# Kernel tuning notes

Hardware: AMD Instinct MI355X
Metric: run time of the kernel (lower is better)

Reference implementation:

```python
import jax, jax.numpy as jnp
import numpy as np

WS = 7        # window size (cubic)
SHIFT = 3     # shift size (cubic)
NH = 6        # num heads
EPS = 1e-5


def _layernorm(x, g, b):
    m = x.mean(-1, keepdims=True)
    v = ((x - m) ** 2).mean(-1, keepdims=True)
    return (x - m) / jnp.sqrt(v + EPS) * g + b


def _win_partition(x, ws):
    # (B,H,W,T,C) -> (B*nW, ws^3, C)
    B, H, W, T, C = x.shape
    x = x.reshape(B, H // ws, ws, W // ws, ws, T // ws, ws, C)
    return x.transpose(0, 1, 3, 5, 2, 4, 6, 7).reshape(-1, ws * ws * ws, C)


def _win_reverse(w, ws, B, H, W, T):
    # (B*nW, ws^3, C) -> (B,H,W,T,C)
    C = w.shape[-1]
    x = w.reshape(B, H // ws, W // ws, T // ws, ws, ws, ws, C)
    return x.transpose(0, 1, 4, 2, 5, 3, 6, 7).reshape(B, H, W, T, C)


def _rel_index(ws):
    # 3D relative position index, (N, N) int, N = ws^3 (torch.meshgrid default 'ij')
    coords = np.stack(np.meshgrid(np.arange(ws), np.arange(ws), np.arange(ws), indexing='ij'))
    cf = coords.reshape(3, -1)
    rel = (cf[:, :, None] - cf[:, None, :]).transpose(1, 2, 0)
    rel[:, :, 0] += ws - 1
    rel[:, :, 1] += ws - 1
    rel[:, :, 2] += ws - 1
    rel[:, :, 0] *= (2 * ws - 1) ** 2
    rel[:, :, 1] *= (2 * ws - 1)
    return rel.sum(-1)


def _compute_mask(Hp, Wp, Tp, ws, shift):
    img = np.zeros((1, Hp, Wp, Tp, 1), np.float32)
    cnt = 0
    sl = (slice(0, -ws), slice(-ws, -shift), slice(-shift, None))
    for h in sl:
        for w in sl:
            for t in sl:
                img[:, h, w, t, :] = cnt
                cnt += 1
    mw = np.asarray(_win_partition(jnp.asarray(img), ws)).reshape(-1, ws ** 3)  # (nW, N)
    am = mw[:, None, :] - mw[:, :, None]
    return jnp.asarray(np.where(am != 0, -100.0, 0.0).astype(np.float32))


def setup_inputs() -> dict:
    key = jax.random.key(0)
    ks = jax.random.split(key, 10)
    B, Hd, Wd, Td, C = 2, 28, 28, 28, 192
    L = Hd * Wd * Td
    Ch = int(C * 4.0)
    s = 0.02
    inp = {
        'x': jax.random.normal(ks[0], (B, L, C), jnp.float32),
        'mask': _compute_mask(Hd, Wd, Td, WS, SHIFT),
        'gamma1': jnp.ones((C,), jnp.float32),
        'beta1': jnp.zeros((C,), jnp.float32),
        'qkv_w': jax.random.normal(ks[1], (3 * C, C), jnp.float32) * s,
        'qkv_b': jnp.zeros((3 * C,), jnp.float32),
        'rpb_table': jax.random.normal(ks[2], ((2 * WS - 1) ** 3, NH), jnp.float32) * s,
        'proj_w': jax.random.normal(ks[3], (C, C), jnp.float32) * s,
        'proj_b': jnp.zeros((C,), jnp.float32),
        'gamma2': jnp.ones((C,), jnp.float32),
        'beta2': jnp.zeros((C,), jnp.float32),
        'fc1_w': jax.random.normal(ks[4], (Ch, C), jnp.float32) * s,
        'fc1_b': jnp.zeros((Ch,), jnp.float32),
        'fc2_w': jax.random.normal(ks[5], (C, Ch), jnp.float32) * s,
        'fc2_b': jnp.zeros((C,), jnp.float32),
        'H': Hd, 'W': Wd, 'T': Td,
    }
    return inp


def reference(x, mask, gamma1, beta1, qkv_w, qkv_b, rpb_table, proj_w, proj_b,
              gamma2, beta2, fc1_w, fc1_b, fc2_w, fc2_b, H, W, T):
    B, L, C = x.shape
    hd = C // NH
    scale = hd ** -0.5
    shortcut = x

    h1 = _layernorm(x, gamma1, beta1).reshape(B, H, W, T, C)
    # H,W,T are multiples of WS -> no padding; cyclic shift for SW-MSA
    shifted = jnp.roll(h1, (-SHIFT, -SHIFT, -SHIFT), axis=(1, 2, 3))
    xw = _win_partition(shifted, WS)            # (B*nW, N, C)
    Bn, N, _ = xw.shape

    qkv = (xw @ qkv_w.T + qkv_b).reshape(Bn, N, 3, NH, hd).transpose(2, 0, 3, 1, 4)
    q, k, v = qkv[0] * scale, qkv[1], qkv[2]     # (Bn, NH, N, hd)
    attn = jnp.einsum('bhnd,bhmd->bhnm', q, k)   # (Bn, NH, N, N)

    idx = _rel_index(WS)
    bias = rpb_table[idx.reshape(-1)].reshape(N, N, NH).transpose(2, 0, 1)
    attn = attn + bias[None]

    nW = mask.shape[0]
    attn = attn.reshape(Bn // nW, nW, NH, N, N) + mask[None, :, None]
    attn = jax.nn.softmax(attn.reshape(Bn, NH, N, N), axis=-1)

    out = jnp.einsum('bhnm,bhmd->bhnd', attn, v).transpose(0, 2, 1, 3).reshape(Bn, N, C)
    out = out @ proj_w.T + proj_b

    shifted = _win_reverse(out, WS, B, H, W, T)
    xr = jnp.roll(shifted, (SHIFT, SHIFT, SHIFT), axis=(1, 2, 3)).reshape(B, L, C)

    x = shortcut + xr
    h2 = _layernorm(x, gamma2, beta2)
    m = jax.nn.gelu(h2 @ fc1_w.T + fc1_b, approximate=False)
    return x + (m @ fc2_w.T + fc2_b)
```

## Files before the change

kernel.cpp:

```cpp
#include <hip/hip_runtime.h>
#include <hip/hip_bf16.h>

typedef unsigned short u16;
typedef unsigned int u32;
typedef __attribute__((ext_vector_type(8))) short s16x8;
typedef __attribute__((ext_vector_type(4))) float f32x4;

__device__ __forceinline__ u16 f2bf(float f) {
    union { float f; u32 u; } x; x.f = f;
    u32 r = x.u + 0x7fffu + ((x.u >> 16) & 1u);
    return (u16)(r >> 16);
}
__device__ __forceinline__ float bflo(u32 v) {
    union { u32 u; float f; } x; x.u = v << 16; return x.f;
}
__device__ __forceinline__ float bfhi(u32 v) {
    union { u32 u; float f; } x; x.u = v & 0xffff0000u; return x.f;
}
__device__ __forceinline__ u32 cvt_pk_bf16(float a, float b) {
    u32 r;
    asm("v_cvt_pk_bf16_f32 %0, %1, %2" : "=v"(r) : "v"(a), "v"(b));
    return r;
}
__device__ __forceinline__ void gl2lds(const u16* g, u16* l) {
    __builtin_amdgcn_global_load_lds(
        (const __attribute__((address_space(1))) unsigned int*)g,
        (__attribute__((address_space(3))) unsigned int*)l, 16, 0, 0);
}

#define L_TOK 21952
#define C_DIM 192
#define LOG2E 1.4426950408889634f
#define Q2SCALE 0.2550565444463649f
#define BT_STR 352

__global__ __launch_bounds__(256) void cvt_k(const float* __restrict__ s0,
                                             const float* __restrict__ s1,
                                             const float* __restrict__ s2,
                                             const float* __restrict__ s3,
                                             u16* __restrict__ dst)
{
    int i = blockIdx.x * 256 + threadIdx.x;
    float v;
    if (i < 110592) v = s0[i];
    else if (i < 147456) v = s1[i - 110592];
    else if (i < 294912) v = s2[i - 147456];
    else v = s3[i - 294912];
    dst[i] = f2bf(v);
}

__global__ __launch_bounds__(256) void bias48_k(const float* __restrict__ rpb,
                                                u16* __restrict__ biasT)
{
    const int gid = blockIdx.x * 256 + threadIdx.x;
    const int z = gid / 30976;
    const int rem = gid - z * 30976;
    const int m = rem / 88;
    const int n0 = (rem - m * 88) * 4;
    const int hh = z >> 3, wt = z & 7;

    u16 v[4];
    if (m <= 342) {
        const int hm = m / 49, r2 = m - hm * 49, wm = r2 / 7, tm = r2 - wm * 7;
        const int rm = ((wt & 4) ? (hm < 4 ? 1 : 2) : 0) * 9
                     + ((wt & 2) ? (wm < 4 ? 1 : 2) : 0) * 3
                     + ((wt & 1) ? (tm < 4 ? 1 : 2) : 0);
        #pragma unroll
        for (int j = 0; j < 4; j++) {
            const int n = n0 + j;
            float b = -100000.0f;
            if (n <= 342) {
                int hq = n / 49, r1 = n - hq * 49, wq = r1 / 7, tq = r1 - wq * 7;
                int idx = ((hq - hm + 6) * 13 + (wq - wm + 6)) * 13 + (tq - tm + 6);
                b = rpb[idx * 6 + hh];
                int rq = ((wt & 4) ? (hq < 4 ? 1 : 2) : 0) * 9
                       + ((wt & 2) ? (wq < 4 ? 1 : 2) : 0) * 3
                       + ((wt & 1) ? (tq < 4 ? 1 : 2) : 0);
                if (rq != rm) b -= 100.0f;
                b *= LOG2E;
            }
            v[j] = f2bf(b);
        }
    } else {
        const u16 neg = f2bf(-100000.0f);
        v[0] = neg; v[1] = neg; v[2] = neg; v[3] = neg;
    }
    u32 lo = (u32)v[0] | ((u32)v[1] << 16);
    u32 hi = (u32)v[2] | ((u32)v[3] << 16);
    *(uint2*)&biasT[((size_t)z * 352 + m) * BT_STR + n0] = (uint2){lo, hi};
}

template<int MODE>
__global__ __launch_bounds__(256) void ln_k(const float* __restrict__ in,
                                            const float* __restrict__ g,
                                            const float* __restrict__ b,
                                            u16* __restrict__ out)
{
    const int lane = threadIdx.x & 63, wv = threadIdx.x >> 6;
    const int tok = blockIdx.x * 4 + wv;
    size_t base = (size_t)tok * C_DIM;
    float x0 = in[base + lane];
    float x1 = in[base + 64 + lane];
    float x2 = in[base + 128 + lane];
    float s = x0 + x1 + x2;
    float sq = x0 * x0 + x1 * x1 + x2 * x2;
    #pragma unroll
    for (int off = 32; off > 0; off >>= 1) {
        s += __shfl_xor(s, off, 64);
        sq += __shfl_xor(sq, off, 64);
    }
    const float mean = s * (1.0f / 192.0f);
    float var = sq * (1.0f / 192.0f) - mean * mean;
    var = fmaxf(var, 0.0f);
    const float rstd = rsqrtf(var + 1e-5f);

    size_t obase;
    if (MODE == 0) {
        int bi = tok / L_TOK;
        int l = tok - bi * L_TOK;
        int h = l / 784;
        int rm = l - h * 784;
        int w = rm / 28;
        int t = rm - w * 28;
        int hs = h + 25; if (hs >= 28) hs -= 28;
        int ws = w + 25; if (ws >= 28) ws -= 28;
        int ts = t + 25; if (ts >= 28) ts -= 28;
        int win = ((bi * 4 + hs / 7) * 4 + ws / 7) * 4 + ts / 7;
        int n = (hs % 7) * 49 + (ws % 7) * 7 + (ts % 7);
        obase = ((size_t)win * 343 + n) * C_DIM;
    } else {
        obase = base;
    }
    #pragma unroll
    for (int i = 0; i < 3; i++) {
        int c = lane + i * 64;
        float xv = (i == 0) ? x0 : (i == 1) ? x1 : x2;
        float y = (xv - mean) * rstd * g[c] + b[c];
        out[obase + c] = f2bf(y);
    }
}

template<int K, int EPI>
__global__ __launch_bounds__(256) void gemm_k(const u16* __restrict__ A,
                                              const u16* __restrict__ W,
                                              const float* __restrict__ bias,
                                              void* __restrict__ outp,
                                              const void* __restrict__ resp,
                                              int Ncols)
{
    __shared__ __align__(16) u16 As[3 * 128 * 32];
    __shared__ __align__(16) u16 Bs[3 * 64 * 32];
    const int t = threadIdx.x;
    const int bm = blockIdx.y;
    const int n0 = blockIdx.x * 64;
    const int lane = t & 63, wv = t >> 6;
    const int wm = (wv >> 1) * 64, wn = (wv & 1) * 32;
    const int r16 = lane & 15, quad = lane >> 4;

    f32x4 acc[4][2];
    #pragma unroll
    for (int i = 0; i < 4; i++)
        #pragma unroll
        for (int j = 0; j < 2; j++) acc[i][j] = (f32x4){0.f, 0.f, 0.f, 0.f};

    const int ar = t >> 2, ac = (t & 3) * 8;
    const size_t abase = (size_t)bm * 128 * K;

    for (int kc = 0; kc < K; kc += 96) {
        if (kc) __syncthreads();
        #pragma unroll
        for (int kt = 0; kt < 3; kt++) {
            const int k0 = kc + kt * 32;
            gl2lds(&A[abase + (size_t)ar * K + k0 + ac], &As[kt * 4096 + 8 * t]);
            gl2lds(&A[abase + (size_t)(ar + 64) * K + k0 + ac], &As[kt * 4096 + 2048 + 8 * t]);
            gl2lds(&W[(size_t)(n0 + ar) * K + k0 + ac], &Bs[kt * 2048 + 8 * t]);
        }
        __syncthreads();
        #pragma unroll
        for (int kt = 0; kt < 3; kt++) {
            s16x8 af[4], bf[2];
            #pragma unroll
            for (int fm = 0; fm < 4; fm++)
                af[fm] = *(const s16x8*)&As[kt * 4096 + (wm + fm * 16 + r16) * 32 + quad * 8];
            #pragma unroll
            for (int fn = 0; fn < 2; fn++)
                bf[fn] = *(const s16x8*)&Bs[kt * 2048 + (wn + fn * 16 + r16) * 32 + quad * 8];
            #pragma unroll
            for (int fm = 0; fm < 4; fm++)
                #pragma unroll
                for (int fn = 0; fn < 2; fn++)
                    acc[fm][fn] = __builtin_amdgcn_mfma_f32_16x16x32_bf16(af[fm], bf[fn], acc[fm][fn], 0, 0, 0);
        }
    }

    #pragma unroll
    for (int fm = 0; fm < 4; fm++) {
        #pragma unroll
        for (int fn = 0; fn < 2; fn++) {
            #pragma unroll
            for (int r = 0; r < 4; r++) {
                const int grow = bm * 128 + wm + fm * 16 + quad * 4 + r;
                const int gcol = n0 + wn + fn * 16 + r16;
                float v = acc[fm][fn][r] + bias[gcol];
                if (EPI == 0) {
                    if (gcol < 192) v *= Q2SCALE;
                    ((u16*)outp)[(size_t)grow * Ncols + gcol] = f2bf(v);
                } else if (EPI == 1) {
                    v = 0.5f * v * (1.0f + erff(v * 0.70710678118654752f));
                    ((u16*)outp)[(size_t)grow * Ncols + gcol] = f2bf(v);
                } else if (EPI == 2) {
                    size_t o = (size_t)grow * C_DIM + gcol;
                    ((float*)outp)[o] = v + ((const float*)resp)[o];
                } else {
                    int win = grow / 343, n = grow - win * 343;
                    int bi = win >> 6, wi = win & 63;
                    int hw = wi >> 4, ww = (wi >> 2) & 3, tw = wi & 3;
                    int ph = n / 49, rem = n - ph * 49;
                    int pw = rem / 7, pt = rem - pw * 7;
                    int h = hw * 7 + ph + 3; if (h >= 28) h -= 28;
                    int w = ww * 7 + pw + 3; if (w >= 28) w -= 28;
                    int tt = tw * 7 + pt + 3; if (tt >= 28) tt -= 28;
                    int l = (h * 28 + w) * 28 + tt;
                    size_t o = ((size_t)bi * L_TOK + l) * C_DIM + gcol;
                    ((float*)outp)[o] = v + ((const float*)resp)[o];
                }
            }
        }
    }
}

__global__ __launch_bounds__(256, 3) void attn_k(const u16* __restrict__ qkv,
                                                 const u16* __restrict__ biasAll,
                                                 u16* __restrict__ out)
{
    __shared__ __align__(16) u16 Ks[352 * 32];
    __shared__ __align__(16) u16 Vt[32 * 360];
    __shared__ __align__(16) u16 Pb[4][16 * 40];

    const int hh = blockIdx.x;
    const int win = blockIdx.y;
    const int wi = win & 63;
    const int t = threadIdx.x, lane = t & 63, wv = t >> 6;
    const int r16 = lane & 15, quad = lane >> 4;
    const size_t qbase = (size_t)win * 343 * 576 + hh * 32;

    for (int j = t; j < 343 * 4; j += 256) {
        int m = j >> 2, ch = j & 3;
        *(uint4*)&Ks[m * 32 + ch * 8] = *(const uint4*)&qkv[qbase + (size_t)m * 576 + 192 + ch * 8];
    }
    if (t < 36) {
        int m = 343 + (t >> 2), ch = t & 3;
        *(uint4*)&Ks[m * 32 + ch * 8] = (uint4){0u, 0u, 0u, 0u};
    }
    for (int i = t; i < 343 * 16; i += 256) {
        int m = i >> 4, d2 = (i & 15) * 2;
        int pm = (m & ~31) + 2 * (m & 15) + ((m >> 4) & 1);
        u32 w2 = *(const u32*)&qkv[qbase + (size_t)m * 576 + 384 + d2];
        Vt[d2 * 360 + pm] = (u16)(w2 & 0xffffu);
        Vt[(d2 + 1) * 360 + pm] = (u16)(w2 >> 16);
    }
    for (int i = t; i < 32 * 9; i += 256) {
        int d = i / 9, m = 343 + i % 9;
        int pm = (m & ~31) + 2 * (m & 15) + ((m >> 4) & 1);
        Vt[d * 360 + pm] = 0;
    }
    __syncthreads();

    const int wt = (((wi >> 4) == 3) ? 4 : 0) | ((((wi >> 2) & 3) == 3) ? 2 : 0)
                 | (((wi & 3) == 3) ? 1 : 0);
    const u16* biashT = biasAll + (size_t)(hh * 8 + wt) * 352 * BT_STR;

    s16x8 onesb;
    #pragma unroll
    for (int j = 0; j < 8; j++) onesb[j] = (short)0x3f80;

    for (int qt = 0; qt < 6; qt++) {
        const int row0 = qt * 64 + wv * 16;
        if (row0 > 342) continue;
        int qrow = row0 + r16; if (qrow > 342) qrow = 342;
        s16x8 qa = *(const s16x8*)&qkv[qbase + (size_t)qrow * 576 + quad * 8];

        const int n0 = row0 + quad * 4;

        f32x4 sacc[22];
        #pragma unroll
        for (int fn = 0; fn < 22; fn++) {
            const int col = fn * 16 + r16;
            uint2 bv = *(const uint2*)&biashT[(size_t)col * BT_STR + n0];
            sacc[fn][0] = bflo(bv.x);
            sacc[fn][1] = bfhi(bv.x);
            sacc[fn][2] = bflo(bv.y);
            sacc[fn][3] = bfhi(bv.y);
        }
        #pragma unroll
        for (int fn = 0; fn < 22; fn++) {
            s16x8 kb = *(const s16x8*)&Ks[(fn * 16 + r16) * 32 + quad * 8];
            sacc[fn] = __builtin_amdgcn_mfma_f32_16x16x32_bf16(qa, kb, sacc[fn], 0, 0, 0);
        }

        #pragma unroll
        for (int fn = 0; fn < 22; fn++) {
            #pragma unroll
            for (int r = 0; r < 4; r++)
                sacc[fn][r] = exp2f(fminf(sacc[fn][r], 42.0f));
        }

        u16* pw = &Pb[wv][0];
        u32* pw32 = (u32*)pw;
        f32x4 oacc0 = (f32x4){0.f, 0.f, 0.f, 0.f};
        f32x4 oacc1 = (f32x4){0.f, 0.f, 0.f, 0.f};
        f32x4 osum  = (f32x4){0.f, 0.f, 0.f, 0.f};
        #pragma unroll
        for (int c = 0; c < 11; c++) {
            asm volatile("s_waitcnt lgkmcnt(0)" ::: "memory");
            #pragma unroll
            for (int r = 0; r < 4; r++)
                pw32[(quad * 4 + r) * 20 + r16] = cvt_pk_bf16(sacc[2 * c][r], sacc[2 * c + 1][r]);
            asm volatile("s_waitcnt lgkmcnt(0)" ::: "memory");
            s16x8 pa = *(const s16x8*)&pw[r16 * 40 + quad * 8];
            s16x8 vb0 = *(const s16x8*)&Vt[r16 * 360 + c * 32 + quad * 8];
            s16x8 vb1 = *(const s16x8*)&Vt[(16 + r16) * 360 + c * 32 + quad * 8];
            oacc0 = __builtin_amdgcn_mfma_f32_16x16x32_bf16(pa, vb0, oacc0, 0, 0, 0);
            oacc1 = __builtin_amdgcn_mfma_f32_16x16x32_bf16(pa, vb1, oacc1, 0, 0, 0);
            osum  = __builtin_amdgcn_mfma_f32_16x16x32_bf16(pa, onesb, osum, 0, 0, 0);
        }

        #pragma unroll
        for (int r = 0; r < 4; r++) {
            const int n = n0 + r;
            if (n < 343) {
                const float rs = osum[r];
                const float inv = rs > 0.0f ? 1.0f / rs : 0.0f;
                size_t o = ((size_t)win * 343 + n) * C_DIM + hh * 32;
                out[o + r16] = f2bf(oacc0[r] * inv);
                out[o + 16 + r16] = f2bf(oacc1[r] * inv);
            }
        }
    }
}

extern "C" void kernel_launch(void* const* d_in, const int* in_sizes, int n_in,
                              void* d_out, int out_size, void* d_ws, size_t ws_size,
                              hipStream_t stream)
{
    const float* x      = (const float*)d_in[0];
    const float* g1     = (const float*)d_in[2];
    const float* b1     = (const float*)d_in[3];
    const float* qkv_w  = (const float*)d_in[4];
    const float* qkv_b  = (const float*)d_in[5];
    const float* rpb    = (const float*)d_in[6];
    const float* proj_w = (const float*)d_in[7];
    const float* proj_b = (const float*)d_in[8];
    const float* g2     = (const float*)d_in[9];
    const float* b2     = (const float*)d_in[10];
    const float* fc1_w  = (const float*)d_in[11];
    const float* fc1_b  = (const float*)d_in[12];
    const float* fc2_w  = (const float*)d_in[13];
    const float* fc2_b  = (const float*)d_in[14];

    char* ws = (char*)d_ws;
    u16* xw        = (u16*)(ws + 0);
    u16* biasT     = (u16*)(ws + 0);
    u16* qkv       = (u16*)(ws + 16861184);
    u16* a1        = (u16*)(ws + 0);
    u16* attn_out  = (u16*)(ws + 67444736);
    u16* h2        = attn_out;
    float* x2      = (float*)(ws + 84305920);
    u16* wbf       = (u16*)(ws + 118028288);
    u16* qkv_wb = wbf;
    u16* proj_wb = wbf + 110592;
    u16* fc1_wb = wbf + 147456;
    u16* fc2_wb = wbf + 294912;

    cvt_k<<<dim3(1728), 256, 0, stream>>>(qkv_w, proj_w, fc1_w, fc2_w, wbf);
    ln_k<0><<<dim3(10976), 256, 0, stream>>>(x, g1, b1, xw);
    gemm_k<192, 0><<<dim3(9, 343), 256, 0, stream>>>(xw, qkv_wb, qkv_b, qkv, nullptr, 576);
    bias48_k<<<dim3(5808), 256, 0, stream>>>(rpb, biasT);
    attn_k<<<dim3(6, 128), 256, 0, stream>>>(qkv, biasT, attn_out);
    gemm_k<192, 3><<<dim3(3, 343), 256, 0, stream>>>(attn_out, proj_wb, proj_b, x2, x, 192);
    ln_k<1><<<dim3(10976), 256, 0, stream>>>(x2, g2, b2, h2);
    gemm_k<192, 1><<<dim3(12, 343), 256, 0, stream>>>(h2, fc1_wb, fc1_b, a1, nullptr, 768);
    gemm_k<768, 2><<<dim3(3, 343), 256, 0, stream>>>(a1, fc2_wb, fc2_b, d_out, x2, 192);
}
```

Before: 345.6 us.

## Replace 128x64 GEMM tile with 64x64 tile and higher occupancy

Swaps the 128x64 block tile (each wave computing 64x32) for a 64x64 tile where each of the 4 waves computes a 16x64 strip, with K staged in 64-wide chunks instead of 96. This doubles the grid and cuts registers and LDS per block, and launch bounds request 8 blocks per CU to improve occupancy and load balance. In exchange there is less reuse per loaded A/B fragment, more LDS traffic per MFMA, and more barrier rounds per K. The epilogue also computes the row address once per row instead of per element.

Result: no change. 343.0 us (-0.7%).

```diff
diff --git a/kernel.cpp b/kernel.cpp
--- a/kernel.cpp
+++ b/kernel.cpp
@@ -141,89 +141,77 @@
 }
 
 template<int K, int EPI>
-__global__ __launch_bounds__(256) void gemm_k(const u16* __restrict__ A,
-                                              const u16* __restrict__ W,
-                                              const float* __restrict__ bias,
-                                              void* __restrict__ outp,
-                                              const void* __restrict__ resp,
-                                              int Ncols)
-{
-    __shared__ __align__(16) u16 As[3 * 128 * 32];
-    __shared__ __align__(16) u16 Bs[3 * 64 * 32];
+__global__ __launch_bounds__(256, 8) void gemm64_k(const u16* __restrict__ A,
+                                                   const u16* __restrict__ W,
+                                                   const float* __restrict__ bias,
+                                                   void* __restrict__ outp,
+                                                   const void* __restrict__ resp,
+                                                   int Ncols)
+{
+    __shared__ __align__(16) u16 As[2 * 2048];
+    __shared__ __align__(16) u16 Bs[2 * 2048];
     const int t = threadIdx.x;
     const int bm = blockIdx.y;
     const int n0 = blockIdx.x * 64;
     const int lane = t & 63, wv = t >> 6;
-    const int wm = (wv >> 1) * 64, wn = (wv & 1) * 32;
     const int r16 = lane & 15, quad = lane >> 4;
-
-    f32x4 acc[4][2];
-    #pragma unroll
-    for (int i = 0; i < 4; i++)
-        #pragma unroll
-        for (int j = 0; j < 2; j++) acc[i][j] = (f32x4){0.f, 0.f, 0.f, 0.f};
-
     const int ar = t >> 2, ac = (t & 3) * 8;
-    const size_t abase = (size_t)bm * 128 * K;
-
-    for (int kc = 0; kc < K; kc += 96) {
+    const size_t abase = (size_t)bm * 64 * K;
+
+    f32x4 acc[4];
+    #pragma unroll
+    for (int fn = 0; fn < 4; fn++) acc[fn] = (f32x4){0.f, 0.f, 0.f, 0.f};
+
+    for (int kc = 0; kc < K; kc += 64) {
         if (kc) __syncthreads();
         #pragma unroll
-        for (int kt = 0; kt < 3; kt++) {
-            const int k0 = kc + kt * 32;
-            gl2lds(&A[abase + (size_t)ar * K + k0 + ac], &As[kt * 4096 + 8 * t]);
-            gl2lds(&A[abase + (size_t)(ar + 64) * K + k0 + ac], &As[kt * 4096 + 2048 + 8 * t]);
-            gl2lds(&W[(size_t)(n0 + ar) * K + k0 + ac], &Bs[kt * 2048 + 8 * t]);
+        for (int kt = 0; kt < 2; kt++) {
+            gl2lds(&A[abase + (size_t)ar * K + kc + kt * 32 + ac], &As[kt * 2048 + 8 * t]);
+            gl2lds(&W[(size_t)(n0 + ar) * K + kc + kt * 32 + ac], &Bs[kt * 2048 + 8 * t]);
         }
         __syncthreads();
         #pragma unroll
-        for (int kt = 0; kt < 3; kt++) {
-            s16x8 af[4], bf[2];
+        for (int kt = 0; kt < 2; kt++) {
+            s16x8 af = *(const s16x8*)&As[kt * 2048 + (wv * 16 + r16) * 32 + quad * 8];
             #pragma unroll
-            for (int fm = 0; fm < 4; fm++)
-                af[fm] = *(const s16x8*)&As[kt * 4096 + (wm + fm * 16 + r16) * 32 + quad * 8];
-            #pragma unroll
-            for (int fn = 0; fn < 2; fn++)
-                bf[fn] = *(const s16x8*)&Bs[kt * 2048 + (wn + fn * 16 + r16) * 32 + quad * 8];
-            #pragma unroll
-            for (int fm = 0; fm < 4; fm++)
-                #pragma unroll
-                for (int fn = 0; fn < 2; fn++)
-                    acc[fm][fn] = __builtin_amdgcn_mfma_f32_16x16x32_bf16(af[fm], bf[fn], acc[fm][fn], 0, 0, 0);
-        }
-    }
-
-    #pragma unroll
-    for (int fm = 0; fm < 4; fm++) {
-        #pragma unroll
-        for (int fn = 0; fn < 2; fn++) {
-            #pragma unroll
-            for (int r = 0; r < 4; r++) {
-                const int grow = bm * 128 + wm + fm * 16 + quad * 4 + r;
-                const int gcol = n0 + wn + fn * 16 + r16;
-                float v = acc[fm][fn][r] + bias[gcol];
-                if (EPI == 0) {
-                    if (gcol < 192) v *= Q2SCALE;
-                    ((u16*)outp)[(size_t)grow * Ncols + gcol] = f2bf(v);
-                } else if (EPI == 1) {
-                    v = 0.5f * v * (1.0f + erff(v * 0.70710678118654752f));
-                    ((u16*)outp)[(size_t)grow * Ncols + gcol] = f2bf(v);
-                } else if (EPI == 2) {
-                    size_t o = (size_t)grow * C_DIM + gcol;
-                    ((float*)outp)[o] = v + ((const float*)resp)[o];
-                } else {
-                    int win = grow / 343, n = grow - win * 343;
-                    int bi = win >> 6, wi = win & 63;
-                    int hw = wi >> 4, ww = (wi >> 2) & 3, tw = wi & 3;
-                    int ph = n / 49, rem = n - ph * 49;
-                    int pw = rem / 7, pt = rem - pw * 7;
-                    int h = hw * 7 + ph + 3; if (h >= 28) h -= 28;
-                    int w = ww * 7 + pw + 3; if (w >= 28) w -= 28;
-                    int tt = tw * 7 + pt + 3; if (tt >= 28) tt -= 28;
-                    int l = (h * 28 + w) * 28 + tt;
-                    size_t o = ((size_t)bi * L_TOK + l) * C_DIM + gcol;
-                    ((float*)outp)[o] = v + ((const float*)resp)[o];
-                }
+            for (int fn = 0; fn < 4; fn++) {
+                s16x8 bf = *(const s16x8*)&Bs[kt * 2048 + (fn * 16 + r16) * 32 + quad * 8];
+                acc[fn] = __builtin_amdgcn_mfma_f32_16x16x32_bf16(af, bf, acc[fn], 0, 0, 0);
+            }
+        }
+    }
+
+    #pragma unroll
+    for (int r = 0; r < 4; r++) {
+        const int grow = bm * 64 + wv * 16 + quad * 4 + r;
+        size_t rowbase;
+        if (EPI == 3) {
+            int win = grow / 343, n = grow - win * 343;
+            int bi = win >> 6, wi = win & 63;
+            int hw = wi >> 4, ww = (wi >> 2) & 3, tw = wi & 3;
+            int ph = n / 49, rem = n - ph * 49;
+            int pw = rem / 7, pt = rem - pw * 7;
+            int h = hw * 7 + ph + 3; if (h >= 28) h -= 28;
+            int w = ww * 7 + pw + 3; if (w >= 28) w -= 28;
+            int tt = tw * 7 + pt + 3; if (tt >= 28) tt -= 28;
+            int l = (h * 28 + w) * 28 + tt;
+            rowbase = ((size_t)bi * L_TOK + l) * C_DIM;
+        } else {
+            rowbase = (size_t)grow * ((EPI == 2) ? C_DIM : Ncols);
+        }
+        #pragma unroll
+        for (int fn = 0; fn < 4; fn++) {
+            const int gcol = n0 + fn * 16 + r16;
+            float v = acc[fn][r] + bias[gcol];
+            if (EPI == 0) {
+                if (gcol < 192) v *= Q2SCALE;
+                ((u16*)outp)[rowbase + gcol] = f2bf(v);
+            } else if (EPI == 1) {
+                v = 0.5f * v * (1.0f + erff(v * 0.70710678118654752f));
+                ((u16*)outp)[rowbase + gcol] = f2bf(v);
+            } else {
+                size_t o = rowbase + gcol;
+                ((float*)outp)[o] = v + ((const float*)resp)[o];
             }
         }
     }
@@ -374,11 +362,11 @@
 
     cvt_k<<<dim3(1728), 256, 0, stream>>>(qkv_w, proj_w, fc1_w, fc2_w, wbf);
     ln_k<0><<<dim3(10976), 256, 0, stream>>>(x, g1, b1, xw);
-    gemm_k<192, 0><<<dim3(9, 343), 256, 0, stream>>>(xw, qkv_wb, qkv_b, qkv, nullptr, 576);
+    gemm64_k<192, 0><<<dim3(9, 686), 256, 0, stream>>>(xw, qkv_wb, qkv_b, qkv, nullptr, 576);
     bias48_k<<<dim3(5808), 256, 0, stream>>>(rpb, biasT);
     attn_k<<<dim3(6, 128), 256, 0, stream>>>(qkv, biasT, attn_out);
-    gemm_k<192, 3><<<dim3(3, 343), 256, 0, stream>>>(attn_out, proj_wb, proj_b, x2, x, 192);
+    gemm64_k<192, 3><<<dim3(3, 686), 256, 0, stream>>>(attn_out, proj_wb, proj_b, x2, x, 192);
     ln_k<1><<<dim3(10976), 256, 0, stream>>>(x2, g2, b2, h2);
-    gemm_k<192, 1><<<dim3(12, 343), 256, 0, stream>>>(h2, fc1_wb, fc1_b, a1, nullptr, 768);
-    gemm_k<768, 2><<<dim3(3, 343), 256, 0, stream>>>(a1, fc2_wb, fc2_b, d_out, x2, 192);
-}
+    gemm64_k<192, 1><<<dim3(12, 686), 256, 0, stream>>>(h2, fc1_wb, fc1_b, a1, nullptr, 768);
+    gemm64_k<768, 2><<<dim3(3, 686), 256, 0, stream>>>(a1, fc2_wb, fc2_b, d_out, x2, 192);
+}
```
